# Performance work log

Hardware: AMD Instinct MI355X
Metric: run time of the kernel (lower is better)

Reference implementation:

```python
import jax, jax.numpy as jnp
import numpy as np

N_NODES = 50000
N_EDGES = 800000
D_FEAT = 100


def setup_inputs() -> dict:
    key = jax.random.key(0)
    ks = jax.random.split(key, 10)
    s = 0.1
    x = jax.random.normal(ks[0], (N_NODES, D_FEAT), dtype=jnp.float32)
    edge_index = jax.random.randint(ks[1], (2, N_EDGES), 0, N_NODES, dtype=jnp.int32)
    return {
        "x": x,
        "edge_index": edge_index,
        "convW0": jax.random.normal(ks[2], (100, 100), jnp.float32) * s,
        "convb0": jnp.zeros((100,), jnp.float32),
        "convW1": jax.random.normal(ks[3], (100, 100), jnp.float32) * s,
        "convb1": jnp.zeros((100,), jnp.float32),
        "linW0": jax.random.normal(ks[4], (100, 10), jnp.float32) * s,
        "linb0": jnp.zeros((10,), jnp.float32),
        "linW1": jax.random.normal(ks[5], (10, 1), jnp.float32) * s,
        "linb1": jnp.zeros((1,), jnp.float32),
    }


def _gcn_conv(x, W, b, src, dst, n):
    """PyG GCNConv: h = x @ W; out[i] = sum_{(j->i)} d_j^{-1/2} d_i^{-1/2} h[j] + b,
    with self-loops already included in (src, dst)."""
    h = x @ W  # [N, out]
    deg = jax.ops.segment_sum(jnp.ones(src.shape[0], x.dtype), dst, num_segments=n)
    dinv = jnp.where(deg > 0, jax.lax.rsqrt(deg), jnp.zeros_like(deg))
    norm = dinv[src] * dinv[dst]  # [E_tot]
    msg = norm[:, None] * h[src]  # gather [E_tot, out]
    out = jax.ops.segment_sum(msg, dst, num_segments=n)  # scatter-add
    return out + b


def reference(x, edge_index, convW0, convb0, convW1, convb1, linW0, linb0, linW1, linb1):
    n = x.shape[0]
    # global-norm division (x.div(torch.norm(x).detach()))
    nm = jax.lax.stop_gradient(jnp.linalg.norm(x))
    x = x / nm
    # NOTE: original re-assigns x via sklearn SelectKBest(chi2, k=100) on raw data.x;
    # that is non-differentiable data preprocessing, so we assume x already holds the
    # k=100 selected features.
    loops = jnp.arange(n, dtype=edge_index.dtype)
    src = jnp.concatenate([edge_index[0], loops])  # self-loops appended
    dst = jnp.concatenate([edge_index[1], loops])
    x = _gcn_conv(x, convW0, convb0, src, dst, n)
    x = _gcn_conv(x, convW1, convb1, src, dst, n)
    # MLP head: ReLU between layers, no activation after the last (loop breaks)
    x = jax.nn.relu(x @ linW0 + linb0)
    x = x @ linW1 + linb1
    return x.T  # [1, N]
```

## Files before the change

### kernel.cpp

```cpp
#include <hip/hip_runtime.h>

#define NN 50000
#define NE 800000
#define ELLW 64

__device__ __forceinline__ float wredf(float v) {
    #pragma unroll
    for (int o = 32; o > 0; o >>= 1) v += __shfl_down(v, o, 64);
    return v;
}

__global__ __launch_bounds__(256) void k_fill(
    const int* __restrict__ src, const int* __restrict__ dst,
    int* __restrict__ cursor, int* __restrict__ ell)
{
    int e = blockIdx.x * 256 + threadIdx.x;
    int s = src[e];
    int d = dst[e];
    int p = atomicAdd(&cursor[d], 1);
    if (p < ELLW) ell[d * ELLW + p] = s;
}

__global__ __launch_bounds__(256) void k_proj(
    const float* __restrict__ x,
    const float* __restrict__ W0, const float* __restrict__ W1,
    const float* __restrict__ cb0, const float* __restrict__ cb1,
    const float* __restrict__ L0, const float* __restrict__ lb0,
    const int* __restrict__ cursor, float* __restrict__ acc,
    float* __restrict__ uvec, float* __restrict__ cvec,
    float* __restrict__ gp)
{
    __shared__ float WA[1000];
    int t = threadIdx.x;
    for (int o = t; o < 1000; o += 256) {
        int j = o / 10, m = o % 10;
        float s = 0.f;
        for (int k = 0; k < 100; ++k) s += W1[j * 100 + k] * L0[k * 10 + m];
        WA[o] = s;
    }
    __syncthreads();
    if (blockIdx.x == 196) {
        if (t < 10) {
            float su = 0.f, scv = 0.f;
            for (int k = 0; k < 100; ++k) {
                su  += cb0[k] * WA[k * 10 + t];
                scv += cb1[k] * L0[k * 10 + t];
            }
            uvec[t] = su;
            cvec[t] = scv + lb0[t];
        }
        return;
    }
    __shared__ float wz[1000];
    for (int o = t; o < 1000; o += 256) {
        int i = o / 10, m = o % 10;
        float s = 0.f;
        for (int k = 0; k < 100; ++k) s += W0[i * 100 + k] * WA[k * 10 + m];
        wz[o] = s;
    }
    __syncthreads();
    int i = blockIdx.x * 256 + t;
    float ss = 0.f;
    float h[10];
    #pragma unroll
    for (int m = 0; m < 10; ++m) h[m] = 0.f;
    if (i < NN) {
        const float4* r4 = (const float4*)(x + i * 100);
        for (int kk = 0; kk < 25; ++kk) {
            float4 a = r4[kk];
            ss += a.x * a.x + a.y * a.y + a.z * a.z + a.w * a.w;
            #pragma unroll
            for (int j = 0; j < 4; ++j) {
                float av = ((const float*)&a)[j];
                int k = kk * 4 + j;
                #pragma unroll
                for (int m = 0; m < 10; ++m) h[m] += av * wz[k * 10 + m];
            }
        }
    }
    ss = wredf(ss);
    __shared__ float p[4];
    if ((t & 63) == 0) p[t >> 6] = ss;
    __syncthreads();
    if (t == 0) atomicAdd(acc, p[0] + p[1] + p[2] + p[3]);

    if (i < NN) {
        float dv = rsqrtf((float)(cursor[i] + 1));
        float o16[16];
        #pragma unroll
        for (int m = 0; m < 10; ++m) o16[m] = dv * h[m];
        o16[10] = dv;
        o16[11] = o16[12] = o16[13] = o16[14] = o16[15] = 0.f;
        float4* dst4 = (float4*)(gp + i * 16);
        #pragma unroll
        for (int q = 0; q < 4; ++q) dst4[q] = *(float4*)&o16[q * 4];
    } else if (i == NN) {
        float4 z = {0.f, 0.f, 0.f, 0.f};
        float4* d4 = (float4*)(gp + NN * 16);
        d4[0] = z; d4[1] = z; d4[2] = z; d4[3] = z;
    }
}

__global__ __launch_bounds__(256) void k_agg1(
    const float* __restrict__ gp, const int* __restrict__ cursor,
    const int* __restrict__ ell, const float* __restrict__ acc,
    float* __restrict__ tb)
{
    int n = (blockIdx.x * 256 + threadIdx.x) >> 6;
    int l = threadIdx.x & 63, g = l >> 4, lane16 = l & 15;
    if (n > NN) return;
    if (n == NN) {
        if (l < 16) tb[NN * 16 + lane16] = 0.f;
        return;
    }
    int rpl = ell[n * ELLW + l];
    int deg = cursor[n];
    int lim = min(deg, ELLW);
    float dvn = rsqrtf((float)(deg + 1));
    float a0 = (g == 0) ? gp[n * 16 + lane16] : 0.f;
    float a1 = 0.f, a2 = 0.f, a3 = 0.f;
    int nq = (lim + 3) >> 2;
    int q = 0;
    for (; q + 4 <= nq; q += 4) {
        int s0 = 4 * q + g;
        int v0 = __shfl(rpl, s0,      64);
        int v1 = __shfl(rpl, s0 + 4,  64);
        int v2 = __shfl(rpl, s0 + 8,  64);
        int v3 = __shfl(rpl, s0 + 12, 64);
        int i0 = (s0      < lim) ? v0 : NN;
        int i1 = (s0 + 4  < lim) ? v1 : NN;
        int i2 = (s0 + 8  < lim) ? v2 : NN;
        int i3 = (s0 + 12 < lim) ? v3 : NN;
        a0 += gp[i0 * 16 + lane16];
        a1 += gp[i1 * 16 + lane16];
        a2 += gp[i2 * 16 + lane16];
        a3 += gp[i3 * 16 + lane16];
    }
    for (; q < nq; ++q) {
        int s0 = 4 * q + g;
        int v0 = __shfl(rpl, s0, 64);
        int i0 = (s0 < lim) ? v0 : NN;
        a0 += gp[i0 * 16 + lane16];
    }
    float s = (a0 + a1) + (a2 + a3);
    s += __shfl_xor(s, 16, 64);
    s += __shfl_xor(s, 32, 64);
    if (l < 16) {
        float sc = rsqrtf(*acc);
        float o = (lane16 < 10) ? sc * dvn * dvn * s
                                : (lane16 == 10 ? dvn * s : 0.f);
        tb[n * 16 + lane16] = o;
    }
}

__global__ __launch_bounds__(256) void k_agg2(
    const float* __restrict__ tb, const int* __restrict__ cursor,
    const int* __restrict__ ell, const float* __restrict__ uvec,
    const float* __restrict__ cvec, const float* __restrict__ L1,
    const float* __restrict__ lb1, float* __restrict__ out)
{
    __shared__ float su[10], scv[10], sl[10];
    if (threadIdx.x < 10) {
        su[threadIdx.x]  = uvec[threadIdx.x];
        scv[threadIdx.x] = cvec[threadIdx.x];
        sl[threadIdx.x]  = L1[threadIdx.x];
    }
    __syncthreads();
    int n = (blockIdx.x * 256 + threadIdx.x) >> 6;
    int l = threadIdx.x & 63, g = l >> 4, lane16 = l & 15;
    int rpl = ell[n * ELLW + l];
    int deg = cursor[n];
    int lim = min(deg, ELLW);
    float dvn = rsqrtf((float)(deg + 1));
    float a0 = (g == 0) ? tb[n * 16 + lane16] : 0.f;
    float a1 = 0.f, a2 = 0.f, a3 = 0.f;
    int nq = (lim + 3) >> 2;
    int q = 0;
    for (; q + 4 <= nq; q += 4) {
        int s0 = 4 * q + g;
        int v0 = __shfl(rpl, s0,      64);
        int v1 = __shfl(rpl, s0 + 4,  64);
        int v2 = __shfl(rpl, s0 + 8,  64);
        int v3 = __shfl(rpl, s0 + 12, 64);
        int i0 = (s0      < lim) ? v0 : NN;
        int i1 = (s0 + 4  < lim) ? v1 : NN;
        int i2 = (s0 + 8  < lim) ? v2 : NN;
        int i3 = (s0 + 12 < lim) ? v3 : NN;
        a0 += tb[i0 * 16 + lane16];
        a1 += tb[i1 * 16 + lane16];
        a2 += tb[i2 * 16 + lane16];
        a3 += tb[i3 * 16 + lane16];
    }
    for (; q < nq; ++q) {
        int s0 = 4 * q + g;
        int v0 = __shfl(rpl, s0, 64);
        int i0 = (s0 < lim) ? v0 : NN;
        a0 += tb[i0 * 16 + lane16];
    }
    float s = (a0 + a1) + (a2 + a3);
    s += __shfl_xor(s, 16, 64);
    s += __shfl_xor(s, 32, 64);
    if (l < 16) {
        float v = tb[n * 16 + 10];
        float hidden = 0.f;
        if (lane16 < 10)
            hidden = fmaxf(dvn * s + v * su[lane16] + scv[lane16], 0.f) * sl[lane16];
        #pragma unroll
        for (int o = 8; o; o >>= 1) hidden += __shfl_down(hidden, o, 16);
        if (lane16 == 0) out[n] = hidden + lb1[0];
    }
}

extern "C" void kernel_launch(void* const* d_in, const int* in_sizes, int n_in,
                              void* d_out, int out_size, void* d_ws, size_t ws_size,
                              hipStream_t stream) {
    const float* x   = (const float*)d_in[0];
    const int*   ei  = (const int*)d_in[1];
    const int*   src = ei;
    const int*   dst = ei + NE;
    const float* W0  = (const float*)d_in[2];
    const float* cb0 = (const float*)d_in[3];
    const float* W1  = (const float*)d_in[4];
    const float* cb1 = (const float*)d_in[5];
    const float* lw0 = (const float*)d_in[6];
    const float* lb0 = (const float*)d_in[7];
    const float* lw1 = (const float*)d_in[8];
    const float* lb1 = (const float*)d_in[9];
    float* out = (float*)d_out;

    char* ws = (char*)d_ws;
    float* acc   = (float*)(ws + 0);
    int*   cursor= (int*)  (ws + 256);
    const size_t zspan = 200320;
    float* uvec  = (float*)(ws + 200448);
    float* cvec  = (float*)(ws + 200576);
    int*   ell   = (int*)  (ws + 200704);
    float* gp    = (float*)(ws + 13000704);
    float* tb    = (float*)(ws + 16200768);

    hipMemsetAsync(d_ws, 0, zspan, stream);
    k_fill <<<3125, 256, 0, stream>>>(src, dst, cursor, ell);
    k_proj <<<197, 256, 0, stream>>>(x, W0, W1, cb0, cb1, lw0, lb0,
                                     cursor, acc, uvec, cvec, gp);
    k_agg1 <<<12501, 256, 0, stream>>>(gp, cursor, ell, acc, tb);
    k_agg2 <<<12500, 256, 0, stream>>>(tb, cursor, ell, uvec, cvec, lw1, lb1, out);
}
```

Baseline: 188.0 us.

## Split projection rows across 4 lanes and batch 4 nodes per wave in aggregation

The projection kernel now assigns four threads per node, each handling a slice of the 100 input features, then reduces the partial 10-wide results with xor shuffles, which quadruples the block count to raise occupancy for the x read. The two aggregation kernels now have each wavefront process four consecutive nodes, prefetching their ELL rows, self features and degrees up front. The neighbour loop is restructured into 16-edge batches. This aims to increase memory-level parallelism and amortise per-node setup. It adds shuffle overhead, and some wavefronts may sit idle on the per-node degree imbalance across the four nodes. Out-of-range reads for n0+3 at the tail rely on workspace slack.

Result: slower. 230.5 us (+22.6%).

```diff
diff --git a/kernel.cpp b/kernel.cpp
--- a/kernel.cpp
+++ b/kernel.cpp
@@ -39,7 +39,7 @@
         WA[o] = s;
     }
     __syncthreads();
-    if (blockIdx.x == 196) {
+    if (blockIdx.x == 784) {
         if (t < 10) {
             float su = 0.f, scv = 0.f;
             for (int k = 0; k < 100; ++k) {
@@ -59,14 +59,17 @@
         wz[o] = s;
     }
     __syncthreads();
-    int i = blockIdx.x * 256 + t;
+    int i = blockIdx.x * 64 + (t >> 2);
+    int sub = t & 3;
+    int k0 = (sub == 0) ? 0 : 7 + (sub - 1) * 6;
+    int k1 = k0 + ((sub == 0) ? 7 : 6);
     float ss = 0.f;
     float h[10];
     #pragma unroll
     for (int m = 0; m < 10; ++m) h[m] = 0.f;
     if (i < NN) {
         const float4* r4 = (const float4*)(x + i * 100);
-        for (int kk = 0; kk < 25; ++kk) {
+        for (int kk = k0; kk < k1; ++kk) {
             float4 a = r4[kk];
             ss += a.x * a.x + a.y * a.y + a.z * a.z + a.w * a.w;
             #pragma unroll
@@ -78,26 +81,33 @@
             }
         }
     }
+    #pragma unroll
+    for (int m = 0; m < 10; ++m) {
+        h[m] += __shfl_xor(h[m], 1, 64);
+        h[m] += __shfl_xor(h[m], 2, 64);
+    }
     ss = wredf(ss);
     __shared__ float p[4];
     if ((t & 63) == 0) p[t >> 6] = ss;
     __syncthreads();
     if (t == 0) atomicAdd(acc, p[0] + p[1] + p[2] + p[3]);
 
-    if (i < NN) {
-        float dv = rsqrtf((float)(cursor[i] + 1));
-        float o16[16];
-        #pragma unroll
-        for (int m = 0; m < 10; ++m) o16[m] = dv * h[m];
-        o16[10] = dv;
-        o16[11] = o16[12] = o16[13] = o16[14] = o16[15] = 0.f;
-        float4* dst4 = (float4*)(gp + i * 16);
-        #pragma unroll
-        for (int q = 0; q < 4; ++q) dst4[q] = *(float4*)&o16[q * 4];
-    } else if (i == NN) {
-        float4 z = {0.f, 0.f, 0.f, 0.f};
-        float4* d4 = (float4*)(gp + NN * 16);
-        d4[0] = z; d4[1] = z; d4[2] = z; d4[3] = z;
+    if (sub == 0) {
+        if (i < NN) {
+            float dv = rsqrtf((float)(cursor[i] + 1));
+            float o16[16];
+            #pragma unroll
+            for (int m = 0; m < 10; ++m) o16[m] = dv * h[m];
+            o16[10] = dv;
+            o16[11] = o16[12] = o16[13] = o16[14] = o16[15] = 0.f;
+            float4* dst4 = (float4*)(gp + i * 16);
+            #pragma unroll
+            for (int q = 0; q < 4; ++q) dst4[q] = *(float4*)&o16[q * 4];
+        } else if (i == NN) {
+            float4 z = {0.f, 0.f, 0.f, 0.f};
+            float4* d4 = (float4*)(gp + NN * 16);
+            d4[0] = z; d4[1] = z; d4[2] = z; d4[3] = z;
+        }
     }
 }
 
@@ -106,50 +116,58 @@
     const int* __restrict__ ell, const float* __restrict__ acc,
     float* __restrict__ tb)
 {
-    int n = (blockIdx.x * 256 + threadIdx.x) >> 6;
+    int w = (blockIdx.x * 256 + threadIdx.x) >> 6;
     int l = threadIdx.x & 63, g = l >> 4, lane16 = l & 15;
-    if (n > NN) return;
-    if (n == NN) {
-        if (l < 16) tb[NN * 16 + lane16] = 0.f;
-        return;
-    }
-    int rpl = ell[n * ELLW + l];
-    int deg = cursor[n];
-    int lim = min(deg, ELLW);
-    float dvn = rsqrtf((float)(deg + 1));
-    float a0 = (g == 0) ? gp[n * 16 + lane16] : 0.f;
-    float a1 = 0.f, a2 = 0.f, a3 = 0.f;
-    int nq = (lim + 3) >> 2;
-    int q = 0;
-    for (; q + 4 <= nq; q += 4) {
-        int s0 = 4 * q + g;
-        int v0 = __shfl(rpl, s0,      64);
-        int v1 = __shfl(rpl, s0 + 4,  64);
-        int v2 = __shfl(rpl, s0 + 8,  64);
-        int v3 = __shfl(rpl, s0 + 12, 64);
-        int i0 = (s0      < lim) ? v0 : NN;
-        int i1 = (s0 + 4  < lim) ? v1 : NN;
-        int i2 = (s0 + 8  < lim) ? v2 : NN;
-        int i3 = (s0 + 12 < lim) ? v3 : NN;
-        a0 += gp[i0 * 16 + lane16];
-        a1 += gp[i1 * 16 + lane16];
-        a2 += gp[i2 * 16 + lane16];
-        a3 += gp[i3 * 16 + lane16];
-    }
-    for (; q < nq; ++q) {
-        int s0 = 4 * q + g;
-        int v0 = __shfl(rpl, s0, 64);
-        int i0 = (s0 < lim) ? v0 : NN;
-        a0 += gp[i0 * 16 + lane16];
-    }
-    float s = (a0 + a1) + (a2 + a3);
-    s += __shfl_xor(s, 16, 64);
-    s += __shfl_xor(s, 32, 64);
-    if (l < 16) {
-        float sc = rsqrtf(*acc);
-        float o = (lane16 < 10) ? sc * dvn * dvn * s
-                                : (lane16 == 10 ? dvn * s : 0.f);
-        tb[n * 16 + lane16] = o;
+    int n0 = w * 4;
+    int rpl0 = ell[(n0 + 0) * ELLW + l];
+    int rpl1 = ell[(n0 + 1) * ELLW + l];
+    int rpl2 = ell[(n0 + 2) * ELLW + l];
+    int rpl3 = ell[(n0 + 3) * ELLW + l];
+    float sf0 = gp[(n0 + 0) * 16 + lane16];
+    float sf1 = gp[(n0 + 1) * 16 + lane16];
+    float sf2 = gp[(n0 + 2) * 16 + lane16];
+    float sf3 = gp[(n0 + 3) * 16 + lane16];
+    int cval = cursor[n0 + (l & 3)];
+    float sc = rsqrtf(*acc);
+    #pragma unroll
+    for (int j = 0; j < 4; ++j) {
+        int n = n0 + j;
+        if (n > NN) continue;
+        if (n == NN) {
+            if (l < 16) tb[NN * 16 + lane16] = 0.f;
+            continue;
+        }
+        int rpl  = (j == 0) ? rpl0 : (j == 1) ? rpl1 : (j == 2) ? rpl2 : rpl3;
+        float sf = (j == 0) ? sf0  : (j == 1) ? sf1  : (j == 2) ? sf2  : sf3;
+        int deg = __shfl(cval, j, 64);
+        int lim = min(deg, ELLW);
+        float dvn = rsqrtf((float)(deg + 1));
+        float a0 = (g == 0) ? sf : 0.f;
+        float a1 = 0.f, a2 = 0.f, a3 = 0.f;
+        int nb = (lim + 15) >> 4;
+        for (int b = 0; b < nb; ++b) {
+            int s0 = b * 16 + g;
+            int v0 = __shfl(rpl, s0,      64);
+            int v1 = __shfl(rpl, s0 + 4,  64);
+            int v2 = __shfl(rpl, s0 + 8,  64);
+            int v3 = __shfl(rpl, s0 + 12, 64);
+            int i0 = (s0      < lim) ? v0 : NN;
+            int i1 = (s0 + 4  < lim) ? v1 : NN;
+            int i2 = (s0 + 8  < lim) ? v2 : NN;
+            int i3 = (s0 + 12 < lim) ? v3 : NN;
+            a0 += gp[i0 * 16 + lane16];
+            a1 += gp[i1 * 16 + lane16];
+            a2 += gp[i2 * 16 + lane16];
+            a3 += gp[i3 * 16 + lane16];
+        }
+        float s = (a0 + a1) + (a2 + a3);
+        s += __shfl_xor(s, 16, 64);
+        s += __shfl_xor(s, 32, 64);
+        if (l < 16) {
+            float o = (lane16 < 10) ? sc * dvn * dvn * s
+                                    : (lane16 == 10 ? dvn * s : 0.f);
+            tb[n * 16 + lane16] = o;
+        }
     }
 }
 
@@ -166,48 +184,58 @@
         sl[threadIdx.x]  = L1[threadIdx.x];
     }
     __syncthreads();
-    int n = (blockIdx.x * 256 + threadIdx.x) >> 6;
+    int w = (blockIdx.x * 256 + threadIdx.x) >> 6;
     int l = threadIdx.x & 63, g = l >> 4, lane16 = l & 15;
-    int rpl = ell[n * ELLW + l];
-    int deg = cursor[n];
-    int lim = min(deg, ELLW);
-    float dvn = rsqrtf((float)(deg + 1));
-    float a0 = (g == 0) ? tb[n * 16 + lane16] : 0.f;
-    float a1 = 0.f, a2 = 0.f, a3 = 0.f;
-    int nq = (lim + 3) >> 2;
-    int q = 0;
-    for (; q + 4 <= nq; q += 4) {
-        int s0 = 4 * q + g;
-        int v0 = __shfl(rpl, s0,      64);
-        int v1 = __shfl(rpl, s0 + 4,  64);
-        int v2 = __shfl(rpl, s0 + 8,  64);
-        int v3 = __shfl(rpl, s0 + 12, 64);
-        int i0 = (s0      < lim) ? v0 : NN;
-        int i1 = (s0 + 4  < lim) ? v1 : NN;
-        int i2 = (s0 + 8  < lim) ? v2 : NN;
-        int i3 = (s0 + 12 < lim) ? v3 : NN;
-        a0 += tb[i0 * 16 + lane16];
-        a1 += tb[i1 * 16 + lane16];
-        a2 += tb[i2 * 16 + lane16];
-        a3 += tb[i3 * 16 + lane16];
-    }
-    for (; q < nq; ++q) {
-        int s0 = 4 * q + g;
-        int v0 = __shfl(rpl, s0, 64);
-        int i0 = (s0 < lim) ? v0 : NN;
-        a0 += tb[i0 * 16 + lane16];
-    }
-    float s = (a0 + a1) + (a2 + a3);
-    s += __shfl_xor(s, 16, 64);
-    s += __shfl_xor(s, 32, 64);
-    if (l < 16) {
-        float v = tb[n * 16 + 10];
-        float hidden = 0.f;
-        if (lane16 < 10)
-            hidden = fmaxf(dvn * s + v * su[lane16] + scv[lane16], 0.f) * sl[lane16];
-        #pragma unroll
-        for (int o = 8; o; o >>= 1) hidden += __shfl_down(hidden, o, 16);
-        if (lane16 == 0) out[n] = hidden + lb1[0];
+    int n0 = w * 4;
+    int rpl0 = ell[(n0 + 0) * ELLW + l];
+    int rpl1 = ell[(n0 + 1) * ELLW + l];
+    int rpl2 = ell[(n0 + 2) * ELLW + l];
+    int rpl3 = ell[(n0 + 3) * ELLW + l];
+    float sf0 = tb[(n0 + 0) * 16 + lane16];
+    float sf1 = tb[(n0 + 1) * 16 + lane16];
+    float sf2 = tb[(n0 + 2) * 16 + lane16];
+    float sf3 = tb[(n0 + 3) * 16 + lane16];
+    int cval = cursor[n0 + (l & 3)];
+    float blb1 = lb1[0];
+    #pragma unroll
+    for (int j = 0; j < 4; ++j) {
+        int n = n0 + j;
+        int rpl  = (j == 0) ? rpl0 : (j == 1) ? rpl1 : (j == 2) ? rpl2 : rpl3;
+        float sf = (j == 0) ? sf0  : (j == 1) ? sf1  : (j == 2) ? sf2  : sf3;
+        int deg = __shfl(cval, j, 64);
+        int lim = min(deg, ELLW);
+        float dvn = rsqrtf((float)(deg + 1));
+        float a0 = (g == 0) ? sf : 0.f;
+        float a1 = 0.f, a2 = 0.f, a3 = 0.f;
+        int nb = (lim + 15) >> 4;
+        for (int b = 0; b < nb; ++b) {
+            int s0 = b * 16 + g;
+            int v0 = __shfl(rpl, s0,      64);
+            int v1 = __shfl(rpl, s0 + 4,  64);
+            int v2 = __shfl(rpl, s0 + 8,  64);
+            int v3 = __shfl(rpl, s0 + 12, 64);
+            int i0 = (s0      < lim) ? v0 : NN;
+            int i1 = (s0 + 4  < lim) ? v1 : NN;
+            int i2 = (s0 + 8  < lim) ? v2 : NN;
+            int i3 = (s0 + 12 < lim) ? v3 : NN;
+            a0 += tb[i0 * 16 + lane16];
+            a1 += tb[i1 * 16 + lane16];
+            a2 += tb[i2 * 16 + lane16];
+            a3 += tb[i3 * 16 + lane16];
+        }
+        float s = (a0 + a1) + (a2 + a3);
+        s += __shfl_xor(s, 16, 64);
+        s += __shfl_xor(s, 32, 64);
+        if (l < 16) {
+            float v = (j == 0) ? __shfl(sf0, 10, 64) : (j == 1) ? __shfl(sf1, 10, 64)
+                     : (j == 2) ? __shfl(sf2, 10, 64) : __shfl(sf3, 10, 64);
+            float hidden = 0.f;
+            if (lane16 < 10)
+                hidden = fmaxf(dvn * s + v * su[lane16] + scv[lane16], 0.f) * sl[lane16];
+            #pragma unroll
+            for (int o = 8; o; o >>= 1) hidden += __shfl_down(hidden, o, 16);
+            if (lane16 == 0) out[n] = hidden + blb1;
+        }
     }
 }
 
@@ -240,8 +268,8 @@
 
     hipMemsetAsync(d_ws, 0, zspan, stream);
     k_fill <<<3125, 256, 0, stream>>>(src, dst, cursor, ell);
-    k_proj <<<197, 256, 0, stream>>>(x, W0, W1, cb0, cb1, lw0, lb0,
+    k_proj <<<785, 256, 0, stream>>>(x, W0, W1, cb0, cb1, lw0, lb0,
                                      cursor, acc, uvec, cvec, gp);
-    k_agg1 <<<12501, 256, 0, stream>>>(gp, cursor, ell, acc, tb);
-    k_agg2 <<<12500, 256, 0, stream>>>(tb, cursor, ell, uvec, cvec, lw1, lb1, out);
-}
+    k_agg1 <<<3126, 256, 0, stream>>>(gp, cursor, ell, acc, tb);
+    k_agg2 <<<3125, 256, 0, stream>>>(tb, cursor, ell, uvec, cvec, lw1, lb1, out);
+}
```
